# Optimization experiments

Hardware: AMD Instinct MI355X
Metric: run time of the kernel (lower is better)

## Reference

```python
import jax, jax.numpy as jnp
import numpy as np

ROUTINGS = 3
NUM_CAPSULE = 32
DIM_CAPSULE = 64
K_EPSILON = 1e-7  # keras K.epsilon()


def squash(x, axis=-1):
    s = jnp.sum(jnp.square(x), axis=axis, keepdims=True) + K_EPSILON
    scale = jnp.sqrt(s) / (0.5 + s)
    return scale * x


def setup_inputs() -> dict:
    key = jax.random.key(0)
    k1, k2 = jax.random.split(key)
    B, N_in, D_in = 32, 1024, 512
    u = jax.random.normal(k1, (B, N_in, D_in), dtype=jnp.float32)
    # glorot_uniform for capsule_kernel (conv1d width-1 kernel == dense matrix)
    fan_out = NUM_CAPSULE * DIM_CAPSULE
    limit = float(np.sqrt(6.0 / (D_in + fan_out)))
    W = jax.random.uniform(k2, (D_in, fan_out), jnp.float32, -limit, limit)
    return {"u": u, "W": W}


def reference(u, W):
    B, N_in, _ = u.shape
    # K.conv1d with width-1 kernel == matmul, then reshape
    u_hat = (u @ W).reshape(B, N_in, NUM_CAPSULE, DIM_CAPSULE)
    u_hat = jnp.transpose(u_hat, (0, 2, 1, 3))  # [B, N_out, N_in, D]
    b = jnp.zeros(u_hat.shape[:3], u_hat.dtype)  # [B, N_out, N_in]
    vj = None
    for i in range(ROUTINGS):
        Wv = jax.nn.softmax(b, axis=1)  # softmax over output capsules (axis=1)
        vj = jnp.einsum('bon,bond->bod', Wv, u_hat)  # batch_dot(Wv,u_hat,[2,2])
        if i < ROUTINGS - 1:
            # K.l2_normalize(vj) with default axis=None -> global L2 norm
            norm = jnp.sqrt(jnp.maximum(jnp.sum(jnp.square(vj)), 1e-12))
            vjn = vj / norm
            b = jnp.einsum('bod,bond->bon', vjn, u_hat)  # batch_dot(vj,u_hat,[2,3])
    return squash(vj)
```

## Files before the change

kernel.cpp:

```cpp
#include <hip/hip_runtime.h>
#include <hip/hip_bf16.h>


constexpr int B = 32, N = 1024, K = 512, O = 32, D = 64, F = 2048;
constexpr int NT = 32;
constexpr int ST = 72;

typedef __attribute__((ext_vector_type(8))) short bf16x8;
typedef __attribute__((ext_vector_type(4))) float f32x4;

__device__ inline unsigned int pk_hi(float x, float y) {
  union { __hip_bfloat162 h; unsigned int u; } c;
  c.h = __float22bfloat162_rn(float2{x, y});
  return c.u;
}
__device__ inline unsigned short bf16_1(float x) {
  return (unsigned short)(pk_hi(x, 0.f) & 0xffffu);
}
__device__ inline void split2(float x, unsigned short& h, unsigned short& l) {
  h = bf16_1(x);
  l = bf16_1(x - __uint_as_float((unsigned int)h << 16));
}
__device__ inline float bf2f(unsigned short h) {
  return __uint_as_float((unsigned int)h << 16);
}
__device__ inline int swz(int r) { return ((r >> 3) & 7) << 3; }

__device__ inline bf16x8 frag_row(const unsigned short* p, int r, int k0) {
  return *(const bf16x8*)&p[r * ST + (k0 ^ swz(r))];
}
__device__ inline bf16x8 frag_col(const unsigned short* p, int c, int n0) {
  bf16x8 f;
#pragma unroll
  for (int j = 0; j < 8; j++) {
    int n = n0 + j;
    f[j] = (short)p[n * ST + (c ^ swz(n))];
  }
  return f;
}

__global__ __launch_bounds__(256) void k_prep(const float* __restrict__ u,
                                              float* __restrict__ cs_part,
                                              unsigned short* __restrict__ u_bf) {
  __shared__ float4 red[128];
  int b = blockIdx.x, ntile = blockIdx.y, n0 = ntile * 32;
  int tid = threadIdx.x;
  int kq = (tid & 127) * 4, ng = tid >> 7;
  const float* ub = u + ((size_t)b * N + n0 + ng * 16) * K + kq;
  unsigned short* ubf = u_bf + ((size_t)b * N + n0 + ng * 16) * K + kq;
  float4 a = {0.f, 0.f, 0.f, 0.f};
#pragma unroll
  for (int nn = 0; nn < 16; nn++) {
    float4 v = *(const float4*)&ub[(size_t)nn * K];
    a.x += v.x; a.y += v.y; a.z += v.z; a.w += v.w;
    uint2 p;
    p.x = pk_hi(v.x, v.y);
    p.y = pk_hi(v.z, v.w);
    *(uint2*)&ubf[(size_t)nn * K] = p;
  }
  if (ng) red[tid & 127] = a;
  __syncthreads();
  if (!ng) {
    float4 o = red[tid];
    float* cs = cs_part + ((size_t)b * 32 + ntile) * K + kq;
    cs[0] = (a.x + o.x) * (1.f / 32.f);
    cs[1] = (a.y + o.y) * (1.f / 32.f);
    cs[2] = (a.z + o.z) * (1.f / 32.f);
    cs[3] = (a.w + o.w) * (1.f / 32.f);
  }
}

__global__ __launch_bounds__(512) void k_vjt(const unsigned short* __restrict__ Sp,
                                             const float* __restrict__ cs_part,
                                             const float* __restrict__ W,
                                             float* __restrict__ ssq_part, int slot,
                                             unsigned short* __restrict__ t_hi,
                                             unsigned short* __restrict__ t_lo) {
  __shared__ __align__(16) float s_s[K];
  __shared__ float red[7][D];
  __shared__ __align__(16) float vs[D];
  int bo = blockIdx.x, b = bo >> 5, o = bo & 31;
  int d = threadIdx.x & 63, ks = threadIdx.x >> 6;
  {
    int i = threadIdx.x;
    float a = 0.f;
    if (slot == 0) {
      const float* base = cs_part + (size_t)b * 32 * K;
#pragma unroll
      for (int nt = 0; nt < 32; nt++) a += base[(size_t)nt * K + i];
    } else {
      const unsigned short* base = Sp + ((size_t)b * NT * O + o) * K;
#pragma unroll
      for (int nt = 0; nt < NT; nt++) a += bf2f(base[(size_t)nt * O * K + i]);
    }
    s_s[i] = a;
  }
  __syncthreads();
  float acc = 0.f;
  const float* Wc = W + (size_t)o * D + d;
  for (int k = ks * 64; k < ks * 64 + 64; k += 4) {
    acc += s_s[k] * Wc[(size_t)k * F] + s_s[k + 1] * Wc[(size_t)(k + 1) * F] +
           s_s[k + 2] * Wc[(size_t)(k + 2) * F] + s_s[k + 3] * Wc[(size_t)(k + 3) * F];
  }
  if (ks) red[ks - 1][d] = acc;
  __syncthreads();
  if (ks == 0) {
#pragma unroll
    for (int j = 0; j < 7; j++) acc += red[j][d];
    vs[d] = acc;
    float ss = acc * acc;
#pragma unroll
    for (int m = 32; m >= 1; m >>= 1) ss += __shfl_xor(ss, m, 64);
    if (d == 0) ssq_part[slot * 1024 + bo] = ss;
  }
  __syncthreads();
  {
    int wave = threadIdx.x >> 6, lane = threadIdx.x & 63;
    int rr = lane >> 3, dc = lane & 7;
    float4 va = *(const float4*)&vs[dc * 8];
    float4 vb = *(const float4*)&vs[dc * 8 + 4];
#pragma unroll
    for (int i = 0; i < 8; i++) {
      int kk = wave * 64 + i * 8 + rr;
      const float* Wr = W + (size_t)kk * F + o * 64 + dc * 8;
      float4 wa = *(const float4*)Wr;
      float4 wb = *(const float4*)(Wr + 4);
      float p = wa.x * va.x + wa.y * va.y + wa.z * va.z + wa.w * va.w +
                wb.x * vb.x + wb.y * vb.y + wb.z * vb.z + wb.w * vb.w;
      p += __shfl_xor(p, 1, 64);
      p += __shfl_xor(p, 2, 64);
      p += __shfl_xor(p, 4, 64);
      if (dc == 0) {
        unsigned short h, l;
        split2(p, h, l);
        t_hi[(size_t)bo * K + kk] = h;
        t_lo[(size_t)bo * K + kk] = l;
      }
    }
  }
}

__global__ __launch_bounds__(512) void k_out(const unsigned short* __restrict__ Sp,
                                             const float* __restrict__ W,
                                             float* __restrict__ out) {
  __shared__ __align__(16) float s_s[K];
  __shared__ float red[7][D];
  int bo = blockIdx.x, b = bo >> 5, o = bo & 31;
  int d = threadIdx.x & 63, ks = threadIdx.x >> 6;
  {
    const unsigned short* base = Sp + ((size_t)b * NT * O + o) * K;
    int i = threadIdx.x;
    float a = 0.f;
#pragma unroll
    for (int nt = 0; nt < NT; nt++) a += bf2f(base[(size_t)nt * O * K + i]);
    s_s[i] = a;
  }
  __syncthreads();
  float acc = 0.f;
  const float* Wc = W + (size_t)o * D + d;
  for (int k = ks * 64; k < ks * 64 + 64; k += 4) {
    acc += s_s[k] * Wc[(size_t)k * F] + s_s[k + 1] * Wc[(size_t)(k + 1) * F] +
           s_s[k + 2] * Wc[(size_t)(k + 2) * F] + s_s[k + 3] * Wc[(size_t)(k + 3) * F];
  }
  if (ks) red[ks - 1][d] = acc;
  __syncthreads();
  if (ks == 0) {
#pragma unroll
    for (int j = 0; j < 7; j++) acc += red[j][d];
    float ss = acc * acc;
#pragma unroll
    for (int m = 32; m >= 1; m >>= 1) ss += __shfl_xor(ss, m, 64);
    float s = ss + 1e-7f;
    out[(size_t)bo * D + d] = (sqrtf(s) / (0.5f + s)) * acc;
  }
}

__global__ __launch_bounds__(256, 4) void k_route(const unsigned short* __restrict__ t_hi_g,
                                                  const unsigned short* __restrict__ t_lo_g,
                                                  const unsigned short* __restrict__ u_bf,
                                                  const float* __restrict__ ssq_part,
                                                  int slot,
                                                  unsigned short* __restrict__ Sp) {
  __shared__ unsigned short u_hi[32 * ST];
  __shared__ unsigned short t_hi[32 * ST], t_lo[32 * ST];
  __shared__ float wv[32 * 36];
  __shared__ float psum[8 * 36];
  __shared__ float mbuf[36];
  unsigned short* wvh = t_hi;
  unsigned short* wvl = t_lo;

  const int b = blockIdx.x, n0 = blockIdx.y * 32;
  const int tid = threadIdx.x, lane = tid & 63, wave = tid >> 6;
  const int m = lane & 15, oct = lane >> 4;
  const unsigned short* ubf = u_bf + ((size_t)b * N + n0) * K;
  const unsigned short* thg = t_hi_g + (size_t)b * O * K;
  const unsigned short* tlg = t_lo_g + (size_t)b * O * K;

  const int sr = tid >> 3, sc8 = (tid & 7) * 8;
  const int scs = sc8 ^ swz(sr);

  const int mo = wave & 1, nt = wave >> 1;
  f32x4 accb = {0.f, 0.f, 0.f, 0.f};
  for (int kc = 0; kc < K; kc += 64) {
    __syncthreads();
    {
      const size_t go = (size_t)sr * K + kc + sc8;
      *(uint4*)&t_hi[sr * ST + scs] = *(const uint4*)&thg[go];
      *(uint4*)&t_lo[sr * ST + scs] = *(const uint4*)&tlg[go];
      *(uint4*)&u_hi[sr * ST + scs] = *(const uint4*)&ubf[go];
    }
    __syncthreads();
#pragma unroll
    for (int ks = 0; ks < 64; ks += 32) {
      bf16x8 ah = frag_row(t_hi, mo * 16 + m, ks + oct * 8);
      bf16x8 al = frag_row(t_lo, mo * 16 + m, ks + oct * 8);
      bf16x8 bh = frag_row(u_hi, nt * 16 + m, ks + oct * 8);
      accb = __builtin_amdgcn_mfma_f32_16x16x32_bf16(ah, bh, accb, 0, 0, 0);
      accb = __builtin_amdgcn_mfma_f32_16x16x32_bf16(al, bh, accb, 0, 0, 0);
    }
  }
  __syncthreads();
  {
    const float* sp = ssq_part + slot * 1024;
    float sa = 0.f;
#pragma unroll
    for (int j = 0; j < 4; j++) sa += sp[tid + j * 256];
    psum[tid & 255] = sa;
    __syncthreads();
    if (tid < 64) {
      float s = psum[tid] + psum[tid + 64] + psum[tid + 128] + psum[tid + 192];
#pragma unroll
      for (int mm = 32; mm >= 1; mm >>= 1) s += __shfl_xor(s, mm, 64);
      if (tid == 0) mbuf[0] = rsqrtf(fmaxf(s, 1e-12f));
    }
    __syncthreads();
  }
  const float nrm_inv = mbuf[0];
  __syncthreads();
#pragma unroll
  for (int r = 0; r < 4; r++)
    wv[(mo * 16 + oct * 4 + r) * 36 + nt * 16 + m] = accb[r] * nrm_inv;
  __syncthreads();

  {
    int n = tid & 31, g = tid >> 5;
    float m4 = -1e30f;
#pragma unroll
    for (int j = 0; j < 4; j++) m4 = fmaxf(m4, wv[(g * 4 + j) * 36 + n]);
    psum[g * 36 + n] = m4;
    __syncthreads();
    if (tid < 32) {
      float mx = psum[tid];
#pragma unroll
      for (int gg = 1; gg < 8; gg++) mx = fmaxf(mx, psum[gg * 36 + tid]);
      mbuf[tid] = mx;
    }
    __syncthreads();
    float mx = mbuf[n];
    float s4 = 0.f;
#pragma unroll
    for (int j = 0; j < 4; j++) {
      float e = __expf(wv[(g * 4 + j) * 36 + n] - mx);
      wv[(g * 4 + j) * 36 + n] = e;
      s4 += e;
    }
    psum[g * 36 + n] = s4;
    __syncthreads();
    if (tid < 32) {
      float s = 0.f;
#pragma unroll
      for (int gg = 0; gg < 8; gg++) s += psum[gg * 36 + tid];
      mbuf[tid] = 1.f / s;
    }
    __syncthreads();
    float inv = mbuf[n];
#pragma unroll
    for (int j = 0; j < 4; j++) {
      unsigned short h, l;
      split2(wv[(g * 4 + j) * 36 + n] * inv, h, l);
      wvh[(g * 4 + j) * ST + n] = h;
      wvl[(g * 4 + j) * ST + n] = l;
    }
  }
  __syncthreads();

  const int mo2 = wave & 1, kp = wave >> 1;
  const int o0 = mo2 * 16;
  bf16x8 a_h = *(const bf16x8*)&wvh[(o0 + m) * ST + oct * 8];
  bf16x8 a_l = *(const bf16x8*)&wvl[(o0 + m) * ST + oct * 8];
  unsigned short* Sb = Sp + ((size_t)b * NT + blockIdx.y) * O * K;
  for (int kc = 0; kc < K; kc += 64) {
    __syncthreads();
    *(uint4*)&u_hi[sr * ST + scs] = *(const uint4*)&ubf[(size_t)sr * K + kc + sc8];
    __syncthreads();
#pragma unroll
    for (int kt = kp * 2; kt < kp * 2 + 2; kt++) {
      int c = kt * 16 + m;
      bf16x8 bh = frag_col(u_hi, c, oct * 8);
      f32x4 acs = {0.f, 0.f, 0.f, 0.f};
      acs = __builtin_amdgcn_mfma_f32_16x16x32_bf16(a_h, bh, acs, 0, 0, 0);
      acs = __builtin_amdgcn_mfma_f32_16x16x32_bf16(a_l, bh, acs, 0, 0, 0);
#pragma unroll
      for (int r = 0; r < 4; r++)
        Sb[(size_t)(o0 + oct * 4 + r) * K + kc + c] = bf16_1(acs[r]);
    }
  }
}

extern "C" void kernel_launch(void* const* d_in, const int* in_sizes, int n_in,
                              void* d_out, int out_size, void* d_ws, size_t ws_size,
                              hipStream_t stream) {
  const float* u = (const float*)d_in[0];
  const float* W = (const float*)d_in[1];
  float* out = (float*)d_out;

  char* ws = (char*)d_ws;
  unsigned short* Sp = (unsigned short*)ws;
  unsigned short* u_bf = Sp + (size_t)B * NT * O * K;
  unsigned short* t_hi = u_bf + (size_t)B * N * K;
  unsigned short* t_lo = t_hi + (size_t)B * O * K;
  float* cs_part = (float*)(t_lo + (size_t)B * O * K);
  float* ssq_part = cs_part + (size_t)B * 32 * K;

  k_prep<<<dim3(B, 32), 256, 0, stream>>>(u, cs_part, u_bf);
  k_vjt<<<B * O, 512, 0, stream>>>(Sp, cs_part, W, ssq_part, 0, t_hi, t_lo);
  k_route<<<dim3(B, NT), 256, 0, stream>>>(t_hi, t_lo, u_bf, ssq_part, 0, Sp);
  k_vjt<<<B * O, 512, 0, stream>>>(Sp, cs_part, W, ssq_part, 1, t_hi, t_lo);
  k_route<<<dim3(B, NT), 256, 0, stream>>>(t_hi, t_lo, u_bf, ssq_part, 1, Sp);
  k_out<<<B * O, 512, 0, stream>>>(Sp, W, out);
}
```

Before: 185.7 us.

## Keep full u tile resident in LDS across both routing phases and prefetch t

k_route now loads the block's whole 32x512 bf16 u tile into shared memory once, instead of streaming it in 64-wide chunks twice (once for the logits GEMM and again for the weighted-sum GEMM). The second phase reuses the resident tile, which drops its per-chunk global loads and barriers. The t_hi/t_lo chunks are register-prefetched one iteration ahead to overlap global latency with MFMA work. LDS use grows to roughly 37KB more per block, so the occupancy hint drops from 4 to 3 blocks per CU.

New measurement: 190.8 us. +2.8%, slower.

```diff
diff --git a/kernel.cpp b/kernel.cpp
--- a/kernel.cpp
+++ b/kernel.cpp
@@ -175,13 +175,13 @@
   }
 }
 
-__global__ __launch_bounds__(256, 4) void k_route(const unsigned short* __restrict__ t_hi_g,
+__global__ __launch_bounds__(256, 3) void k_route(const unsigned short* __restrict__ t_hi_g,
                                                   const unsigned short* __restrict__ t_lo_g,
                                                   const unsigned short* __restrict__ u_bf,
                                                   const float* __restrict__ ssq_part,
                                                   int slot,
                                                   unsigned short* __restrict__ Sp) {
-  __shared__ unsigned short u_hi[32 * ST];
+  __shared__ unsigned short u_res[8][32 * ST];
   __shared__ unsigned short t_hi[32 * ST], t_lo[32 * ST];
   __shared__ float wv[32 * 36];
   __shared__ float psum[8 * 36];
@@ -199,22 +199,31 @@
   const int sr = tid >> 3, sc8 = (tid & 7) * 8;
   const int scs = sc8 ^ swz(sr);
 
+  uint4 rth = *(const uint4*)&thg[(size_t)sr * K + sc8];
+  uint4 rtl = *(const uint4*)&tlg[(size_t)sr * K + sc8];
+#pragma unroll
+  for (int ch = 0; ch < 8; ch++) {
+    *(uint4*)&u_res[ch][sr * ST + scs] =
+        *(const uint4*)&ubf[(size_t)sr * K + ch * 64 + sc8];
+  }
+
   const int mo = wave & 1, nt = wave >> 1;
   f32x4 accb = {0.f, 0.f, 0.f, 0.f};
-  for (int kc = 0; kc < K; kc += 64) {
-    __syncthreads();
-    {
-      const size_t go = (size_t)sr * K + kc + sc8;
-      *(uint4*)&t_hi[sr * ST + scs] = *(const uint4*)&thg[go];
-      *(uint4*)&t_lo[sr * ST + scs] = *(const uint4*)&tlg[go];
-      *(uint4*)&u_hi[sr * ST + scs] = *(const uint4*)&ubf[go];
-    }
-    __syncthreads();
+  for (int kcb = 0; kcb < 8; kcb++) {
+    __syncthreads();
+    *(uint4*)&t_hi[sr * ST + scs] = rth;
+    *(uint4*)&t_lo[sr * ST + scs] = rtl;
+    __syncthreads();
+    if (kcb < 7) {
+      rth = *(const uint4*)&thg[(size_t)sr * K + kcb * 64 + 64 + sc8];
+      rtl = *(const uint4*)&tlg[(size_t)sr * K + kcb * 64 + 64 + sc8];
+    }
+    const unsigned short* uc = u_res[kcb];
 #pragma unroll
     for (int ks = 0; ks < 64; ks += 32) {
       bf16x8 ah = frag_row(t_hi, mo * 16 + m, ks + oct * 8);
       bf16x8 al = frag_row(t_lo, mo * 16 + m, ks + oct * 8);
-      bf16x8 bh = frag_row(u_hi, nt * 16 + m, ks + oct * 8);
+      bf16x8 bh = frag_row(uc, nt * 16 + m, ks + oct * 8);
       accb = __builtin_amdgcn_mfma_f32_16x16x32_bf16(ah, bh, accb, 0, 0, 0);
       accb = __builtin_amdgcn_mfma_f32_16x16x32_bf16(al, bh, accb, 0, 0, 0);
     }
@@ -289,20 +298,18 @@
   bf16x8 a_h = *(const bf16x8*)&wvh[(o0 + m) * ST + oct * 8];
   bf16x8 a_l = *(const bf16x8*)&wvl[(o0 + m) * ST + oct * 8];
   unsigned short* Sb = Sp + ((size_t)b * NT + blockIdx.y) * O * K;
-  for (int kc = 0; kc < K; kc += 64) {
-    __syncthreads();
-    *(uint4*)&u_hi[sr * ST + scs] = *(const uint4*)&ubf[(size_t)sr * K + kc + sc8];
-    __syncthreads();
+  for (int kcb = 0; kcb < 8; kcb++) {
+    const unsigned short* uc = u_res[kcb];
 #pragma unroll
     for (int kt = kp * 2; kt < kp * 2 + 2; kt++) {
       int c = kt * 16 + m;
-      bf16x8 bh = frag_col(u_hi, c, oct * 8);
+      bf16x8 bh = frag_col(uc, c, oct * 8);
       f32x4 acs = {0.f, 0.f, 0.f, 0.f};
       acs = __builtin_amdgcn_mfma_f32_16x16x32_bf16(a_h, bh, acs, 0, 0, 0);
       acs = __builtin_amdgcn_mfma_f32_16x16x32_bf16(a_l, bh, acs, 0, 0, 0);
 #pragma unroll
       for (int r = 0; r < 4; r++)
-        Sb[(size_t)(o0 + oct * 4 + r) * K + kc + c] = bf16_1(acs[r]);
+        Sb[(size_t)(o0 + oct * 4 + r) * K + kcb * 64 + c] = bf16_1(acs[r]);
     }
   }
 }
```
